# Kernel optimization log

Hardware: AMD Instinct MI355X
Metric: run time of the kernel (lower is better)

Reference implementation:

```python
import jax, jax.numpy as jnp
import numpy as np
import math

B, S, D = 2, 2048, 2048
H = 16
DH = D // H  # 128


def setup_inputs() -> dict:
    key = jax.random.key(0)
    ks = jax.random.split(key, 11)
    sd = 1.0 / math.sqrt(D)
    inp = {
        "q": jax.random.normal(ks[0], (B, S, D), jnp.float32),
        "k": jax.random.normal(ks[1], (B, S, D), jnp.float32),
        "v": jax.random.normal(ks[2], (B, S, D), jnp.float32),
        "Wq": jax.random.normal(ks[3], (D, D), jnp.float32) * sd,
        "bq": jnp.zeros((D,), jnp.float32),
        "Wk": jax.random.normal(ks[4], (D, D), jnp.float32) * sd,
        "bk": jnp.zeros((D,), jnp.float32),
        "Wv": jax.random.normal(ks[5], (D, D), jnp.float32) * sd,
        "bv": jnp.zeros((D,), jnp.float32),
        "Wo": jax.random.normal(ks[6], (D, D), jnp.float32) * sd,
        "bo": jnp.zeros((D,), jnp.float32),
        "causal_mask": 1,
    }
    return inp


def _split_heads(x):
    # [b, s, d] -> [b, h, s, dh]
    b, s, _ = x.shape
    return x.reshape(b, s, H, DH).transpose(0, 2, 1, 3)


def reference(q, k, v, Wq, bq, Wk, bk, Wv, bv, Wo, bo, causal_mask):
    b, s, _ = q.shape
    # torch Linear: x @ W.T + b
    qh = _split_heads(q @ Wq.T + bq)
    kh = _split_heads(k @ Wk.T + bk)
    vh = _split_heads(v @ Wv.T + bv)
    # scores [b, h, sq, sk]
    scores = jnp.einsum("bhqd,bhkd->bhqk", qh, kh)
    if causal_mask:
        tri = jnp.triu(jnp.ones((s, s), dtype=bool), k=1)
        scores = jnp.where(tri, -jnp.inf, scores)
    scores = scores / math.sqrt(DH)
    attn = jax.nn.softmax(scores, axis=-1)
    out = jnp.einsum("bhqk,bhkd->bhqd", attn, vh)  # [b, h, s, dh]
    out = out.transpose(0, 2, 1, 3).reshape(b, s, H * DH)
    return out @ Wo.T + bo
```

## Files before the change

### kernel.cpp

```cpp
#include <hip/hip_runtime.h>
#include <hip/hip_bf16.h>

typedef __bf16 bf16_t;
typedef bf16_t bf16x8 __attribute__((ext_vector_type(8)));
typedef bf16_t bf16x4 __attribute__((ext_vector_type(4)));
typedef float  f32x4  __attribute__((ext_vector_type(4)));
typedef float  f32x16 __attribute__((ext_vector_type(16)));
typedef unsigned int u32;
typedef u32 u32x4 __attribute__((ext_vector_type(4)));

#define S_LEN  2048
#define DMODEL 2048
#define NH     16
#define DH     128
#define BATCH  2
#define MROWS  (BATCH * S_LEN)

#define NEG_BIG (-1.0e30f)

__device__ __forceinline__ bf16x8 cvt8_f32_bf16(const float* __restrict__ p) {
  float4 f0 = *(const float4*)(p);
  float4 f1 = *(const float4*)(p + 4);
  bf16x8 r;
  r[0] = (bf16_t)f0.x; r[1] = (bf16_t)f0.y; r[2] = (bf16_t)f0.z; r[3] = (bf16_t)f0.w;
  r[4] = (bf16_t)f1.x; r[5] = (bf16_t)f1.y; r[6] = (bf16_t)f1.z; r[7] = (bf16_t)f1.w;
  return r;
}

__device__ __forceinline__ void gld16(const void* g, void* l) {
  __builtin_amdgcn_global_load_lds(
      (const __attribute__((address_space(1))) void*)g,
      (__attribute__((address_space(3))) void*)l, 16, 0, 0);
}

__device__ __forceinline__ float exp2fast(float x) {
#if __has_builtin(__builtin_amdgcn_exp2f)
  return __builtin_amdgcn_exp2f(x);
#else
  return __expf(x * 0.6931471805599453f);
#endif
}

__device__ __forceinline__ u32 pack_bf16(float lo, float hi) {
  union { bf16_t h[2]; u32 w; } u;
  u.h[0] = (bf16_t)lo; u.h[1] = (bf16_t)hi;
  return u.w;
}

__global__ __launch_bounds__(256)
void cvt_bf16(const float* __restrict__ s, bf16_t* __restrict__ d, int n8) {
  int i = blockIdx.x * 256 + threadIdx.x;
  if (i < n8) *(bf16x8*)(&d[(size_t)i * 8]) = cvt8_f32_bf16(&s[(size_t)i * 8]);
}

template <typename TA, typename TW, typename TC>
__global__ __launch_bounds__(256)
void gemm_bt(const TA* __restrict__ A, const TW* __restrict__ W,
             const float* __restrict__ bias, TC* __restrict__ C,
             int mode, float oscale)
{
  constexpr int K = DMODEL, N = DMODEL;
  __shared__ __align__(16) bf16_t As[128 * 32];
  __shared__ __align__(16) bf16_t Bs[128 * 32];
  const int tid  = threadIdx.x;
  const int wave = tid >> 6, lane = tid & 63;
  const int quad = lane >> 4, l16 = lane & 15;
  const int bm = blockIdx.x * 128, bn = blockIdx.y * 128;
  const int wm = (wave >> 1) * 64, wn = (wave & 1) * 64;

  f32x4 acc[4][4] = {};

  for (int k0 = 0; k0 < K; k0 += 32) {
    __syncthreads();
    if constexpr (__is_same(TA, float)) {
#pragma unroll
      for (int i = 0; i < 2; ++i) {
        int c = tid + i * 256, row = c >> 2, col = (c & 3) << 3;
        *(bf16x8*)(&As[row * 32 + col]) =
            cvt8_f32_bf16(&A[(size_t)(bm + row) * K + k0 + col]);
      }
    } else {
#pragma unroll
      for (int t = 0; t < 2; ++t) {
        int chunk = wave * 128 + t * 64 + lane;
        int row = chunk >> 2, col = (chunk & 3) << 3;
        gld16(&A[(size_t)(bm + row) * K + k0 + col], &As[row * 32 + col]);
      }
    }
    if constexpr (__is_same(TW, float)) {
#pragma unroll
      for (int i = 0; i < 2; ++i) {
        int c = tid + i * 256, row = c >> 2, col = (c & 3) << 3;
        *(bf16x8*)(&Bs[row * 32 + col]) =
            cvt8_f32_bf16(&W[(size_t)(bn + row) * K + k0 + col]);
      }
    } else {
#pragma unroll
      for (int t = 0; t < 2; ++t) {
        int chunk = wave * 128 + t * 64 + lane;
        int row = chunk >> 2, col = (chunk & 3) << 3;
        gld16(&W[(size_t)(bn + row) * K + k0 + col], &Bs[row * 32 + col]);
      }
    }
    __syncthreads();
    bf16x8 af[4], bfr[4];
#pragma unroll
    for (int i = 0; i < 4; ++i) {
      af[i]  = *(const bf16x8*)(&As[(wm + i * 16 + l16) * 32 + quad * 8]);
      bfr[i] = *(const bf16x8*)(&Bs[(wn + i * 16 + l16) * 32 + quad * 8]);
    }
#pragma unroll
    for (int mi = 0; mi < 4; ++mi)
#pragma unroll
      for (int ni = 0; ni < 4; ++ni)
        acc[mi][ni] = __builtin_amdgcn_mfma_f32_16x16x32_bf16(
            af[mi], bfr[ni], acc[mi][ni], 0, 0, 0);
  }

#pragma unroll
  for (int mi = 0; mi < 4; ++mi) {
#pragma unroll
    for (int ni = 0; ni < 4; ++ni) {
      int col = bn + wn + ni * 16 + l16;
      float bval = bias[col];
      if (mode == 2) {
        int row0 = bm + wm + mi * 16 + quad * 4;
        int b = row0 >> 11, s = row0 & (S_LEN - 1);
        int h = col >> 7,  d = col & (DH - 1);
        size_t idx0 = (((size_t)(b * NH + h)) * DH + d) * S_LEN + s;
        if constexpr (__is_same(TC, bf16_t)) {
          bf16x4 o4;
#pragma unroll
          for (int r = 0; r < 4; ++r) o4[r] = (bf16_t)((acc[mi][ni][r] + bval) * oscale);
          *(bf16x4*)(&C[idx0]) = o4;
        } else {
#pragma unroll
          for (int r = 0; r < 4; ++r) C[idx0 + r] = (TC)((acc[mi][ni][r] + bval) * oscale);
        }
      } else {
#pragma unroll
        for (int r = 0; r < 4; ++r) {
          int row = bm + wm + mi * 16 + quad * 4 + r;
          float vv = (acc[mi][ni][r] + bval) * oscale;
          size_t idx;
          if (mode == 0) {
            idx = (size_t)row * N + col;
          } else {
            int b = row >> 11, s = row & (S_LEN - 1);
            int h = col >> 7,  d = col & (DH - 1);
            idx = (((size_t)(b * NH + h)) * S_LEN + s) * DH + d;
          }
          C[idx] = (TC)vv;
        }
      }
    }
  }
}

__global__ __launch_bounds__(256, 2)
void attn_fwd(const bf16_t* __restrict__ Q, const bf16_t* __restrict__ Kh,
              const bf16_t* __restrict__ Vt, bf16_t* __restrict__ O,
              const int* __restrict__ causal_p)
{
  __shared__ __align__(16) bf16_t Ks[2][64 * 128];
  __shared__ __align__(16) bf16_t Vs[2][128 * 64];
  const int tid  = threadIdx.x;
  const int wave = tid >> 6, lane = tid & 63;
  const int l31  = lane & 31, hi = lane >> 5;
  const int id = blockIdx.x;
  const int bh = id & 31;
  const int phase = id >> 5;
  const int qb = (phase < 8) ? (15 - phase) : (phase - 8);
  const int causal = *causal_p;

  const bf16_t* Qb = Q  + (size_t)bh * S_LEN * DH;
  const bf16_t* Kb = Kh + (size_t)bh * S_LEN * DH;
  const bf16_t* Vb = Vt + (size_t)bh * DH * S_LEN;

  const int qrow   = qb * 128 + wave * 32 + l31;
  const int qmin_w = qb * 128 + wave * 32;

  bf16x8 qf[8];
#pragma unroll
  for (int kk = 0; kk < 8; ++kk)
    qf[kk] = *(const bf16x8*)(&Qb[(size_t)qrow * DH + kk * 16 + hi * 8]);

  f32x16 oacc[4] = {};
  float mrow = NEG_BIG, lrow = 0.f;

  const int nkb = causal ? (2 * qb + 2) : (S_LEN / 64);

  auto STAGE = [&](int buf, int kb_) {
#pragma unroll
    for (int i = 0; i < 4; ++i) {
      int c = tid + i * 256;
      int kr = c >> 4, kc = c & 15;
      gld16(&Kb[(size_t)(kb_ * 64 + kr) * DH + ((kc ^ (kr & 7)) << 3)],
            &Ks[buf][c << 3]);
      int vr = c >> 3, vc = c & 7;
      gld16(&Vb[(size_t)vr * S_LEN + kb_ * 64 + ((vc ^ (vr & 7)) << 3)],
            &Vs[buf][c << 3]);
    }
  };

  STAGE(0, 0);
  int cur = 0;
  for (int kb = 0; kb < nkb; ++kb) {
    __syncthreads();
    if (kb + 1 < nkb) STAGE(cur ^ 1, kb + 1);

    if (!causal || (kb * 64 <= qmin_w + 31)) {
      const bf16_t* ks = &Ks[cur][0];
      const bf16_t* vs = &Vs[cur][0];

      f32x16 sc[2] = {};
#pragma unroll
      for (int kk = 0; kk < 8; ++kk) {
        int ch = ((kk << 1) | hi) ^ (l31 & 7);
        bf16x8 kf0 = *(const bf16x8*)(&ks[(l31) * 128 + ch * 8]);
        bf16x8 kf1 = *(const bf16x8*)(&ks[(32 + l31) * 128 + ch * 8]);
        sc[0] = __builtin_amdgcn_mfma_f32_32x32x16_bf16(kf0, qf[kk], sc[0], 0, 0, 0);
        sc[1] = __builtin_amdgcn_mfma_f32_32x32x16_bf16(kf1, qf[kk], sc[1], 0, 0, 0);
      }

      if (causal && (kb * 64 + 63 > qmin_w)) {
#pragma unroll
        for (int kblk = 0; kblk < 2; ++kblk)
#pragma unroll
          for (int r = 0; r < 16; ++r) {
            int key = kb * 64 + kblk * 32 + (r & 3) + 8 * (r >> 2) + 4 * hi;
            if (key > qrow) sc[kblk][r] = NEG_BIG;
          }
      }

      float pm = sc[0][0];
#pragma unroll
      for (int r = 1; r < 16; ++r) pm = fmaxf(pm, sc[0][r]);
#pragma unroll
      for (int r = 0; r < 16; ++r) pm = fmaxf(pm, sc[1][r]);
      pm = fmaxf(pm, __shfl_xor(pm, 32));
      float mnew  = fmaxf(mrow, pm);
      float alpha = exp2fast(mrow - mnew);
      mrow = mnew;
      float rs = 0.f;
#pragma unroll
      for (int kblk = 0; kblk < 2; ++kblk)
#pragma unroll
        for (int r = 0; r < 16; ++r) {
          float e = exp2fast(sc[kblk][r] - mnew);
          sc[kblk][r] = e;
          rs += e;
        }
      rs += __shfl_xor(rs, 32);
      lrow = lrow * alpha + rs;
#pragma unroll
      for (int d = 0; d < 4; ++d) oacc[d] *= alpha;

      u32x4 pw[2][2];
#pragma unroll
      for (int kblk = 0; kblk < 2; ++kblk)
#pragma unroll
        for (int kc = 0; kc < 2; ++kc) {
          int b0 = kc * 8;
          u32 pa = pack_bf16(sc[kblk][b0 + 0], sc[kblk][b0 + 1]);
          u32 pc = pack_bf16(sc[kblk][b0 + 2], sc[kblk][b0 + 3]);
          u32 pb = pack_bf16(sc[kblk][b0 + 4], sc[kblk][b0 + 5]);
          u32 pd = pack_bf16(sc[kblk][b0 + 6], sc[kblk][b0 + 7]);
          u32 qa = (u32)__shfl_xor((int)pa, 32);
          u32 qb_ = (u32)__shfl_xor((int)pb, 32);
          u32 qc = (u32)__shfl_xor((int)pc, 32);
          u32 qd = (u32)__shfl_xor((int)pd, 32);
          u32x4 w;
          w[0] = hi ? qb_ : pa;
          w[1] = hi ? qd  : pc;
          w[2] = hi ? pb  : qa;
          w[3] = hi ? pd  : qc;
          pw[kblk][kc] = w;
        }

#pragma unroll
      for (int d = 0; d < 4; ++d) {
        int vrow = d * 32 + l31;
#pragma unroll
        for (int kblk = 0; kblk < 2; ++kblk)
#pragma unroll
          for (int kc = 0; kc < 2; ++kc) {
            bf16x8 vf = *(const bf16x8*)(
                &vs[vrow * 64 + ((((kblk << 2) | (kc << 1) | hi)) ^ (l31 & 7)) * 8]);
            bf16x8 pf = __builtin_bit_cast(bf16x8, pw[kblk][kc]);
            oacc[d] = __builtin_amdgcn_mfma_f32_32x32x16_bf16(vf, pf, oacc[d], 0, 0, 0);
          }
      }
    }
    cur ^= 1;
  }

  const int b = bh >> 4, h = bh & 15;
  float linv = 1.0f / fmaxf(lrow, 1e-20f);
  bf16_t* Ob = O + ((size_t)(b * S_LEN + qrow)) * DMODEL + h * DH;
#pragma unroll
  for (int d = 0; d < 4; ++d)
#pragma unroll
    for (int g = 0; g < 4; ++g) {
      bf16x4 o4;
#pragma unroll
      for (int j = 0; j < 4; ++j) o4[j] = (bf16_t)(oacc[d][g * 4 + j] * linv);
      *(bf16x4*)(&Ob[d * 32 + g * 8 + hi * 4]) = o4;
    }
}

extern "C" void kernel_launch(void* const* d_in, const int* in_sizes, int n_in,
                              void* d_out, int out_size, void* d_ws, size_t ws_size,
                              hipStream_t stream) {
  const float* q  = (const float*)d_in[0];
  const float* k  = (const float*)d_in[1];
  const float* v  = (const float*)d_in[2];
  const float* Wq = (const float*)d_in[3];
  const float* bq = (const float*)d_in[4];
  const float* Wk = (const float*)d_in[5];
  const float* bk = (const float*)d_in[6];
  const float* Wv = (const float*)d_in[7];
  const float* bv = (const float*)d_in[8];
  const float* Wo = (const float*)d_in[9];
  const float* bo = (const float*)d_in[10];
  const int*   cm = (const int*)d_in[11];

  float* out = (float*)d_out;
  const size_t NA = (size_t)MROWS * DMODEL;
  const size_t NW = (size_t)DMODEL * DMODEL;
  const float qscale = 0.08838834764831845f * 1.4426950408889634f;

  bf16_t* p0 = (bf16_t*)d_ws;
  const size_t needA = (4 * NW + 7 * NA) * sizeof(bf16_t);
  const size_t needB = (4 * NW + 4 * NA) * sizeof(bf16_t);

  dim3 gg(MROWS / 128, DMODEL / 128), bb(256);
  dim3 cgW(2048), cgA(4096);
  dim3 ga(512);
  bf16_t *Qh, *Kh, *Vh, *Ao;

  if (ws_size >= needA) {
    bf16_t *Wqb = p0, *Wkb = p0 + NW, *Wvb = p0 + 2 * NW, *Wob = p0 + 3 * NW;
    bf16_t *qb2 = p0 + 4 * NW, *kb2 = qb2 + NA, *vb2 = kb2 + NA;
    Qh = vb2 + NA; Kh = Qh + NA; Vh = Kh + NA; Ao = Vh + NA;
    cvt_bf16<<<cgW, bb, 0, stream>>>(Wq, Wqb, (int)(NW / 8));
    cvt_bf16<<<cgW, bb, 0, stream>>>(Wk, Wkb, (int)(NW / 8));
    cvt_bf16<<<cgW, bb, 0, stream>>>(Wv, Wvb, (int)(NW / 8));
    cvt_bf16<<<cgW, bb, 0, stream>>>(Wo, Wob, (int)(NW / 8));
    cvt_bf16<<<cgA, bb, 0, stream>>>(q, qb2, (int)(NA / 8));
    cvt_bf16<<<cgA, bb, 0, stream>>>(k, kb2, (int)(NA / 8));
    cvt_bf16<<<cgA, bb, 0, stream>>>(v, vb2, (int)(NA / 8));
    gemm_bt<bf16_t, bf16_t, bf16_t><<<gg, bb, 0, stream>>>(qb2, Wqb, bq, Qh, 1, qscale);
    gemm_bt<bf16_t, bf16_t, bf16_t><<<gg, bb, 0, stream>>>(kb2, Wkb, bk, Kh, 1, 1.0f);
    gemm_bt<bf16_t, bf16_t, bf16_t><<<gg, bb, 0, stream>>>(vb2, Wvb, bv, Vh, 2, 1.0f);
    attn_fwd<<<ga, bb, 0, stream>>>(Qh, Kh, Vh, Ao, cm);
    gemm_bt<bf16_t, bf16_t, float><<<gg, bb, 0, stream>>>(Ao, Wob, bo, out, 0, 1.0f);
  } else if (ws_size >= needB) {
    bf16_t *Wqb = p0, *Wkb = p0 + NW, *Wvb = p0 + 2 * NW, *Wob = p0 + 3 * NW;
    Qh = p0 + 4 * NW; Kh = Qh + NA; Vh = Kh + NA; Ao = Vh + NA;
    cvt_bf16<<<cgW, bb, 0, stream>>>(Wq, Wqb, (int)(NW / 8));
    cvt_bf16<<<cgW, bb, 0, stream>>>(Wk, Wkb, (int)(NW / 8));
    cvt_bf16<<<cgW, bb, 0, stream>>>(Wv, Wvb, (int)(NW / 8));
    cvt_bf16<<<cgW, bb, 0, stream>>>(Wo, Wob, (int)(NW / 8));
    gemm_bt<float, bf16_t, bf16_t><<<gg, bb, 0, stream>>>(q, Wqb, bq, Qh, 1, qscale);
    gemm_bt<float, bf16_t, bf16_t><<<gg, bb, 0, stream>>>(k, Wkb, bk, Kh, 1, 1.0f);
    gemm_bt<float, bf16_t, bf16_t><<<gg, bb, 0, stream>>>(v, Wvb, bv, Vh, 2, 1.0f);
    attn_fwd<<<ga, bb, 0, stream>>>(Qh, Kh, Vh, Ao, cm);
    gemm_bt<bf16_t, bf16_t, float><<<gg, bb, 0, stream>>>(Ao, Wob, bo, out, 0, 1.0f);
  } else {
    Qh = p0; Kh = Qh + NA; Vh = Kh + NA; Ao = Vh + NA;
    gemm_bt<float, float, bf16_t><<<gg, bb, 0, stream>>>(q, Wq, bq, Qh, 1, qscale);
    gemm_bt<float, float, bf16_t><<<gg, bb, 0, stream>>>(k, Wk, bk, Kh, 1, 1.0f);
    gemm_bt<float, float, bf16_t><<<gg, bb, 0, stream>>>(v, Wv, bv, Vh, 2, 1.0f);
    attn_fwd<<<ga, bb, 0, stream>>>(Qh, Kh, Vh, Ao, cm);
    gemm_bt<bf16_t, float, float><<<gg, bb, 0, stream>>>(Ao, Wo, bo, out, 0, 1.0f);
  }
}
```

Before: 463.8 us.

## Load V fragments directly to registers, add MFMA priority hints, batch conversion launches

The attention kernel stops staging V tiles through shared memory. Each lane now loads its V fragments straight from global memory into registers at the start of each key block, and the MFMA sections are wrapped in s_setprio raises. Separately, the seven per-tensor fp32-to-bf16 conversion launches are merged into two multi-tensor kernels to cut launch overhead. The direct V loads are not coalesced as well and are not prefetched a block ahead, and the register footprint grows.

```diff
diff --git a/kernel.cpp b/kernel.cpp
--- a/kernel.cpp
+++ b/kernel.cpp
@@ -48,9 +48,24 @@
 }
 
 __global__ __launch_bounds__(256)
-void cvt_bf16(const float* __restrict__ s, bf16_t* __restrict__ d, int n8) {
-  int i = blockIdx.x * 256 + threadIdx.x;
-  if (i < n8) *(bf16x8*)(&d[(size_t)i * 8]) = cvt8_f32_bf16(&s[(size_t)i * 8]);
+void cvt_bf16_w4(const float* __restrict__ a, const float* __restrict__ b,
+                 const float* __restrict__ c, const float* __restrict__ d,
+                 bf16_t* __restrict__ o, int blocksPer) {
+  int which = blockIdx.x / blocksPer;
+  int j = (blockIdx.x - which * blocksPer) * 256 + threadIdx.x;
+  const float* s = (which == 0) ? a : (which == 1) ? b : (which == 2) ? c : d;
+  bf16_t* dst = o + (size_t)which * ((size_t)blocksPer * 256 * 8);
+  *(bf16x8*)(&dst[(size_t)j * 8]) = cvt8_f32_bf16(&s[(size_t)j * 8]);
+}
+
+__global__ __launch_bounds__(256)
+void cvt_bf16_a3(const float* __restrict__ a, const float* __restrict__ b,
+                 const float* __restrict__ c, bf16_t* __restrict__ o, int blocksPer) {
+  int which = blockIdx.x / blocksPer;
+  int j = (blockIdx.x - which * blocksPer) * 256 + threadIdx.x;
+  const float* s = (which == 0) ? a : (which == 1) ? b : c;
+  bf16_t* dst = o + (size_t)which * ((size_t)blocksPer * 256 * 8);
+  *(bf16x8*)(&dst[(size_t)j * 8]) = cvt8_f32_bf16(&s[(size_t)j * 8]);
 }
 
 template <typename TA, typename TW, typename TC>
@@ -163,7 +178,6 @@
               const int* __restrict__ causal_p)
 {
   __shared__ __align__(16) bf16_t Ks[2][64 * 128];
-  __shared__ __align__(16) bf16_t Vs[2][128 * 64];
   const int tid  = threadIdx.x;
   const int wave = tid >> 6, lane = tid & 63;
   const int l31  = lane & 31, hi = lane >> 5;
@@ -197,9 +211,6 @@
       int kr = c >> 4, kc = c & 15;
       gld16(&Kb[(size_t)(kb_ * 64 + kr) * DH + ((kc ^ (kr & 7)) << 3)],
             &Ks[buf][c << 3]);
-      int vr = c >> 3, vc = c & 7;
-      gld16(&Vb[(size_t)vr * S_LEN + kb_ * 64 + ((vc ^ (vr & 7)) << 3)],
-            &Vs[buf][c << 3]);
     }
   };
 
@@ -211,9 +222,17 @@
 
     if (!causal || (kb * 64 <= qmin_w + 31)) {
       const bf16_t* ks = &Ks[cur][0];
-      const bf16_t* vs = &Vs[cur][0];
+
+      bf16x8 vfr[4][4];
+#pragma unroll
+      for (int d = 0; d < 4; ++d)
+#pragma unroll
+        for (int t = 0; t < 4; ++t)
+          vfr[d][t] = *(const bf16x8*)(
+              &Vb[(size_t)(d * 32 + l31) * S_LEN + kb * 64 + t * 16 + hi * 8]);
 
       f32x16 sc[2] = {};
+      __builtin_amdgcn_s_setprio(1);
 #pragma unroll
       for (int kk = 0; kk < 8; ++kk) {
         int ch = ((kk << 1) | hi) ^ (l31 & 7);
@@ -222,6 +241,7 @@
         sc[0] = __builtin_amdgcn_mfma_f32_32x32x16_bf16(kf0, qf[kk], sc[0], 0, 0, 0);
         sc[1] = __builtin_amdgcn_mfma_f32_32x32x16_bf16(kf1, qf[kk], sc[1], 0, 0, 0);
       }
+      __builtin_amdgcn_s_setprio(0);
 
       if (causal && (kb * 64 + 63 > qmin_w)) {
 #pragma unroll
@@ -278,19 +298,18 @@
           pw[kblk][kc] = w;
         }
 
-#pragma unroll
-      for (int d = 0; d < 4; ++d) {
-        int vrow = d * 32 + l31;
+      __builtin_amdgcn_s_setprio(1);
+#pragma unroll
+      for (int d = 0; d < 4; ++d)
 #pragma unroll
         for (int kblk = 0; kblk < 2; ++kblk)
 #pragma unroll
           for (int kc = 0; kc < 2; ++kc) {
-            bf16x8 vf = *(const bf16x8*)(
-                &vs[vrow * 64 + ((((kblk << 2) | (kc << 1) | hi)) ^ (l31 & 7)) * 8]);
             bf16x8 pf = __builtin_bit_cast(bf16x8, pw[kblk][kc]);
-            oacc[d] = __builtin_amdgcn_mfma_f32_32x32x16_bf16(vf, pf, oacc[d], 0, 0, 0);
+            oacc[d] = __builtin_amdgcn_mfma_f32_32x32x16_bf16(
+                vfr[d][kblk * 2 + kc], pf, oacc[d], 0, 0, 0);
           }
-      }
+      __builtin_amdgcn_s_setprio(0);
     }
     cur ^= 1;
   }
@@ -335,38 +354,33 @@
   const size_t needB = (4 * NW + 4 * NA) * sizeof(bf16_t);
 
   dim3 gg(MROWS / 128, DMODEL / 128), bb(256);
-  dim3 cgW(2048), cgA(4096);
   dim3 ga(512);
   bf16_t *Qh, *Kh, *Vh, *Ao;
 
   if (ws_size >= needA) {
-    bf16_t *Wqb = p0, *Wkb = p0 + NW, *Wvb = p0 + 2 * NW, *Wob = p0 + 3 * NW;
-    bf16_t *qb2 = p0 + 4 * NW, *kb2 = qb2 + NA, *vb2 = kb2 + NA;
+    bf16_t *Wqb = p0;
+    bf16_t *qb2 = p0 + 4 * NW;
+    bf16_t *kb2 = qb2 + NA, *vb2 = kb2 + NA;
     Qh = vb2 + NA; Kh = Qh + NA; Vh = Kh + NA; Ao = Vh + NA;
-    cvt_bf16<<<cgW, bb, 0, stream>>>(Wq, Wqb, (int)(NW / 8));
-    cvt_bf16<<<cgW, bb, 0, stream>>>(Wk, Wkb, (int)(NW / 8));
-    cvt_bf16<<<cgW, bb, 0, stream>>>(Wv, Wvb, (int)(NW / 8));
-    cvt_bf16<<<cgW, bb, 0, stream>>>(Wo, Wob, (int)(NW / 8));
-    cvt_bf16<<<cgA, bb, 0, stream>>>(q, qb2, (int)(NA / 8));
-    cvt_bf16<<<cgA, bb, 0, stream>>>(k, kb2, (int)(NA / 8));
-    cvt_bf16<<<cgA, bb, 0, stream>>>(v, vb2, (int)(NA / 8));
-    gemm_bt<bf16_t, bf16_t, bf16_t><<<gg, bb, 0, stream>>>(qb2, Wqb, bq, Qh, 1, qscale);
-    gemm_bt<bf16_t, bf16_t, bf16_t><<<gg, bb, 0, stream>>>(kb2, Wkb, bk, Kh, 1, 1.0f);
-    gemm_bt<bf16_t, bf16_t, bf16_t><<<gg, bb, 0, stream>>>(vb2, Wvb, bv, Vh, 2, 1.0f);
+    cvt_bf16_w4<<<dim3(4 * (int)(NW / 2048)), bb, 0, stream>>>(
+        Wq, Wk, Wv, Wo, Wqb, (int)(NW / 2048));
+    cvt_bf16_a3<<<dim3(3 * (int)(NA / 2048)), bb, 0, stream>>>(
+        q, k, v, qb2, (int)(NA / 2048));
+    gemm_bt<bf16_t, bf16_t, bf16_t><<<gg, bb, 0, stream>>>(qb2, Wqb,          bq, Qh, 1, qscale);
+    gemm_bt<bf16_t, bf16_t, bf16_t><<<gg, bb, 0, stream>>>(kb2, Wqb + NW,     bk, Kh, 1, 1.0f);
+    gemm_bt<bf16_t, bf16_t, bf16_t><<<gg, bb, 0, stream>>>(vb2, Wqb + 2 * NW, bv, Vh, 2, 1.0f);
     attn_fwd<<<ga, bb, 0, stream>>>(Qh, Kh, Vh, Ao, cm);
-    gemm_bt<bf16_t, bf16_t, float><<<gg, bb, 0, stream>>>(Ao, Wob, bo, out, 0, 1.0f);
+    gemm_bt<bf16_t, bf16_t, float><<<gg, bb, 0, stream>>>(Ao, Wqb + 3 * NW, bo, out, 0, 1.0f);
   } else if (ws_size >= needB) {
-    bf16_t *Wqb = p0, *Wkb = p0 + NW, *Wvb = p0 + 2 * NW, *Wob = p0 + 3 * NW;
+    bf16_t *Wqb = p0;
     Qh = p0 + 4 * NW; Kh = Qh + NA; Vh = Kh + NA; Ao = Vh + NA;
-    cvt_bf16<<<cgW, bb, 0, stream>>>(Wq, Wqb, (int)(NW / 8));
-    cvt_bf16<<<cgW, bb, 0, stream>>>(Wk, Wkb, (int)(NW / 8));
-    cvt_bf16<<<cgW, bb, 0, stream>>>(Wv, Wvb, (int)(NW / 8));
-    cvt_bf16<<<cgW, bb, 0, stream>>>(Wo, Wob, (int)(NW / 8));
-    gemm_bt<float, bf16_t, bf16_t><<<gg, bb, 0, stream>>>(q, Wqb, bq, Qh, 1, qscale);
-    gemm_bt<float, bf16_t, bf16_t><<<gg, bb, 0, stream>>>(k, Wkb, bk, Kh, 1, 1.0f);
-    gemm_bt<float, bf16_t, bf16_t><<<gg, bb, 0, stream>>>(v, Wvb, bv, Vh, 2, 1.0f);
+    cvt_bf16_w4<<<dim3(4 * (int)(NW / 2048)), bb, 0, stream>>>(
+        Wq, Wk, Wv, Wo, Wqb, (int)(NW / 2048));
+    gemm_bt<float, bf16_t, bf16_t><<<gg, bb, 0, stream>>>(q, Wqb,          bq, Qh, 1, qscale);
+    gemm_bt<float, bf16_t, bf16_t><<<gg, bb, 0, stream>>>(k, Wqb + NW,     bk, Kh, 1, 1.0f);
+    gemm_bt<float, bf16_t, bf16_t><<<gg, bb, 0, stream>>>(v, Wqb + 2 * NW, bv, Vh, 2, 1.0f);
     attn_fwd<<<ga, bb, 0, stream>>>(Qh, Kh, Vh, Ao, cm);
-    gemm_bt<bf16_t, bf16_t, float><<<gg, bb, 0, stream>>>(Ao, Wob, bo, out, 0, 1.0f);
+    gemm_bt<bf16_t, bf16_t, float><<<gg, bb, 0, stream>>>(Ao, Wqb + 3 * NW, bo, out, 0, 1.0f);
   } else {
     Qh = p0; Kh = Qh + NA; Vh = Kh + NA; Ao = Vh + NA;
     gemm_bt<float, float, bf16_t><<<gg, bb, 0, stream>>>(q, Wq, bq, Qh, 1, qscale);
```

Measured after the change: 472.9 us. Within noise of the previous version (+2.0%).
